# Optimization experiments

Hardware: AMD Instinct MI355X
Metric: run time of the kernel (lower is better)

## Reference

```python
import jax, jax.numpy as jnp
import numpy as np

N_NODES = 200000
N_EDGES = 6400000
IN_DIM, HID_DIM, OUT_DIM = 32, 32, 16


def setup_inputs() -> dict:
    key = jax.random.key(0)
    kx, ke, k1, k2, k3, k4 = jax.random.split(key, 6)
    x = jax.random.normal(kx, (N_NODES, IN_DIM), dtype=jnp.float32)
    edge_index = jax.random.randint(ke, (2, N_EDGES), 0, N_NODES, dtype=jnp.int32)
    # Glorot-ish init for GCNConv weights, zero bias (PyG default bias=True)
    W1 = jax.random.normal(k1, (IN_DIM, HID_DIM), dtype=jnp.float32) * (1.0 / np.sqrt(IN_DIM))
    b1 = jnp.zeros((HID_DIM,), dtype=jnp.float32)
    W2 = jax.random.normal(k2, (HID_DIM, OUT_DIM), dtype=jnp.float32) * (1.0 / np.sqrt(HID_DIM))
    b2 = jnp.zeros((OUT_DIM,), dtype=jnp.float32)
    return {"x": x, "edge_index": edge_index, "W1": W1, "b1": b1, "W2": W2, "b2": b2}


def reference(x, edge_index, W1, b1, W2, b2):
    n = x.shape[0]
    loops = jnp.arange(n, dtype=edge_index.dtype)
    # PyG GCNConv default: add self-loops, symmetric normalization
    src = jnp.concatenate([edge_index[0], loops])  # message source j
    dst = jnp.concatenate([edge_index[1], loops])  # aggregation target i
    deg = jax.ops.segment_sum(jnp.ones_like(dst, dtype=x.dtype), dst, num_segments=n)
    dinv = jax.lax.rsqrt(deg)  # deg >= 1 thanks to self-loops
    norm = dinv[src] * dinv[dst]  # [E+N]

    def gcn_conv(h, W, b):
        hw = h @ W                                   # [N, F_out] transform first (F_out <= F_in)
        msg = hw[src] * norm[:, None]                # [E+N, F_out] gather + scale
        return jax.ops.segment_sum(msg, dst, num_segments=n) + b

    h1 = jax.nn.relu(gcn_conv(x, W1, b1))
    # dropout p=0.0 is identity
    return gcn_conv(h1, W2, b2)
```

## Files before the change

### kernel.cpp

```cpp
#include <hip/hip_runtime.h>
#include <hip/hip_fp16.h>


#define BN 256
#define NBSZ 800
#define CHUNK 6144
#define KPT (CHUNK / 256)
#define CAPB 9216
#define CAP 12288
#define SRCCH 25000

typedef _Float16 h2f __attribute__((ext_vector_type(2)));

__device__ __forceinline__ h2f u2h(unsigned u) {
    union { unsigned u; h2f h; } x; x.u = u; return x.h;
}
__device__ __forceinline__ float fd2(h2f a, h2f sel, float acc) {
    return __builtin_amdgcn_fdot2(a, sel, acc, false);
}

__global__ __launch_bounds__(256) void init_cursors(int* gcursor, int nb) {
    int i = blockIdx.x * 256 + threadIdx.x;
    if (i < nb) gcursor[i] = i * CAPB;
}

__global__ __launch_bounds__(256) void partition_kernel(
    const int* __restrict__ src, const int* __restrict__ dst, int E,
    int* __restrict__ gcursor, unsigned int* __restrict__ ebuf, int nb) {
    __shared__ int hist[NBSZ];
    __shared__ int cur[NBSZ];
    __shared__ int gbase[NBSZ];
    __shared__ unsigned int sword[CHUNK];
    __shared__ unsigned short sbkt[CHUNK];
    __shared__ int wsum[4];
    __shared__ int totv;
    int tid = threadIdx.x;
    int e0 = blockIdx.x * CHUNK;
    int myd[KPT], mys[KPT];
    for (int k = 0; k < KPT; ++k) {
        int e = e0 + k * 256 + tid;
        myd[k] = (e < E) ? dst[e] : -1;
        mys[k] = (e < E) ? src[e] : 0;
    }
    for (int b = tid; b < nb; b += 256) hist[b] = 0;
    __syncthreads();
    for (int k = 0; k < KPT; ++k) if (myd[k] >= 0) atomicAdd(&hist[myd[k] >> 8], 1);
    __syncthreads();
    {
        int lane = tid & 63, wid = tid >> 6;
        int s0 = tid * 4;
        int local[4]; int part = 0;
        for (int j = 0; j < 4; ++j) { int b = s0 + j; local[j] = (b < nb) ? hist[b] : 0; part += local[j]; }
        int v = part;
        for (int o = 1; o < 64; o <<= 1) { int t = __shfl_up(v, o); if (lane >= o) v += t; }
        if (lane == 63) wsum[wid] = v;
        __syncthreads();
        int woff = 0;
        for (int w = 0; w < wid; ++w) woff += wsum[w];
        int run = woff + v - part;
        for (int j = 0; j < 4; ++j) {
            int b = s0 + j;
            if (b < nb) { hist[b] = run; cur[b] = run; run += local[j]; }
        }
        if (tid == 255) totv = run;
    }
    __syncthreads();
    for (int k = 0; k < KPT; ++k) {
        if (myd[k] >= 0) {
            int b = myd[k] >> 8;
            int r = atomicAdd(&cur[b], 1);
            sword[r] = ((unsigned)mys[k] << 8) | (unsigned)(myd[k] & 255);
            sbkt[r] = (unsigned short)b;
        }
    }
    __syncthreads();
    for (int b = tid; b < nb; b += 256) {
        int c = cur[b] - hist[b];
        if (c) gbase[b] = atomicAdd(&gcursor[b], c);
    }
    __syncthreads();
    int tv = totv;
    for (int i = tid; i < tv; i += 256) {
        int b = sbkt[i];
        ebuf[gbase[b] + (i - hist[b])] = sword[i];
    }
}

__global__ __launch_bounds__(256) void refine_kernel(
    unsigned int* __restrict__ ebuf, const int* __restrict__ gcursor,
    int* __restrict__ node_start, uint2* __restrict__ node_degc,
    float* __restrict__ dinv, int n) {
    __shared__ int cnt[BN * 8];
    __shared__ int cur[BN * 8];
    __shared__ int wsum[4];
    __shared__ int ssrc[CAP];
    int b = blockIdx.x, tid = threadIdx.x;
    int s = b * CAPB;
    int len = gcursor[b] - s;
    for (int i = tid; i < BN * 8; i += 256) cnt[i] = 0;
    __syncthreads();
    for (int i = tid; i < len; i += 256) {
        unsigned int w = ebuf[s + i];
        unsigned int key = ((w & 255u) << 3) | ((w >> 8) / SRCCH);
        atomicAdd(&cnt[key], 1);
    }
    __syncthreads();
    int s0 = tid * 8;
    int local[8]; int part = 0;
#pragma unroll
    for (int j = 0; j < 8; ++j) { local[j] = cnt[s0 + j]; part += local[j]; }
    int v = part;
    int lane = tid & 63, wid = tid >> 6;
    for (int o = 1; o < 64; o <<= 1) { int t = __shfl_up(v, o); if (lane >= o) v += t; }
    if (lane == 63) wsum[wid] = v;
    __syncthreads();
    int woff = 0;
    for (int w = 0; w < wid; ++w) woff += wsum[w];
    int run = woff + v - part;
    int mystart = run;
#pragma unroll
    for (int j = 0; j < 8; ++j) { cnt[s0 + j] = run; cur[s0 + j] = run; run += local[j]; }
    int node = b * BN + tid;
    if (node < n) {
        node_start[node] = s + mystart;
        uint2 dc;
        dc.x = (unsigned)local[0] | ((unsigned)local[1] << 8)
             | ((unsigned)local[2] << 16) | ((unsigned)local[3] << 24);
        dc.y = (unsigned)local[4] | ((unsigned)local[5] << 8)
             | ((unsigned)local[6] << 16) | ((unsigned)local[7] << 24);
        node_degc[node] = dc;
        dinv[node] = rsqrtf((float)part + 1.0f);
    }
    __syncthreads();
    if (len <= CAP) {
        for (int i = tid; i < len; i += 256) {
            unsigned int w = ebuf[s + i];
            unsigned int key = ((w & 255u) << 3) | ((w >> 8) / SRCCH);
            int r = atomicAdd(&cur[key], 1);
            ssrc[r] = (int)(w >> 8);
        }
        __syncthreads();
        for (int i = tid; i < len; i += 256) ebuf[s + i] = (unsigned int)ssrc[i];
    } else {
        for (int i = tid; i < len; i += 256) {
            unsigned int w = ebuf[s + i];
            unsigned int key = ((w & 255u) << 3) | ((w >> 8) / SRCCH);
            int r = atomicAdd(&cur[key], 1);
            ebuf[s + r] = (w >> 8);
        }
    }
}

__global__ __launch_bounds__(256) void transform1(
    const float* __restrict__ x, const float* __restrict__ W1,
    const float* __restrict__ dinv, __half* __restrict__ hws1, int n) {
    __shared__ float sW[32 * 32];
    __shared__ float sx[8 * 32];
    int tid = threadIdx.x;
    for (int i = tid; i < 1024; i += 256) sW[i] = W1[i];
    int node0 = blockIdx.x * 8;
    int node_ld = node0 + tid / 32;
    sx[tid] = (node_ld < n) ? x[node_ld * 32 + (tid & 31)] : 0.0f;
    __syncthreads();
    int local = tid >> 5;
    int f = tid & 31;
    int node = node0 + local;
    if (node >= n) return;
    float acc = 0.0f;
#pragma unroll
    for (int k = 0; k < 32; ++k) acc += sx[local * 32 + k] * sW[k * 32 + f];
    hws1[(size_t)node * 32 + f] = __float2half(acc * dinv[node]);
}

__global__ __launch_bounds__(256) void pull1_fused(
    const int* __restrict__ node_start, const uint2* __restrict__ node_degc,
    const unsigned int* __restrict__ ecsr, const float* __restrict__ dinv,
    const __half* __restrict__ hws1, const float* __restrict__ b1,
    const float* __restrict__ W2, __half* __restrict__ hws2, int n) {
    __shared__ float sW2[32 * 17];
    __shared__ float sb1[32];
    int tid = threadIdx.x;
    for (int i = tid; i < 512; i += 256) sW2[(i >> 4) * 17 + (i & 15)] = W2[i];
    if (tid < 32) sb1[tid] = b1[tid];
    __syncthreads();
    const h2f SEL_LO = {(_Float16)1.0f, (_Float16)0.0f};
    const h2f SEL_HI = {(_Float16)0.0f, (_Float16)1.0f};
    int g = tid >> 2;
    int l = tid & 3;
    int d = blockIdx.x * 64 + g;
    if (d >= n) return;
    int b = node_start[d];
    uint2 dc = node_degc[d];
    const char* Hb = (const char*)hws1;
    unsigned loff = (unsigned)(l << 4);
    float acc[8] = {0, 0, 0, 0, 0, 0, 0, 0};
    {
        uint4 r = *(const uint4*)(Hb + (((unsigned)d << 6) | loff));
        acc[0] = fd2(u2h(r.x), SEL_LO, acc[0]); acc[1] = fd2(u2h(r.x), SEL_HI, acc[1]);
        acc[2] = fd2(u2h(r.y), SEL_LO, acc[2]); acc[3] = fd2(u2h(r.y), SEL_HI, acc[3]);
        acc[4] = fd2(u2h(r.z), SEL_LO, acc[4]); acc[5] = fd2(u2h(r.z), SEL_HI, acc[5]);
        acc[6] = fd2(u2h(r.w), SEL_LO, acc[6]); acc[7] = fd2(u2h(r.w), SEL_HI, acc[7]);
    }
    int off = 0;
#pragma unroll
    for (int c = 0; c < 8; ++c) {
        unsigned int word = (c < 4) ? dc.x : dc.y;
        int lc = (int)((word >> (8 * (c & 3))) & 255u);
        int j = 0;
        for (; j + 4 <= lc; j += 4) {
            unsigned o0 = (ecsr[b + off + j]     << 6) | loff;
            unsigned o1 = (ecsr[b + off + j + 1] << 6) | loff;
            unsigned o2 = (ecsr[b + off + j + 2] << 6) | loff;
            unsigned o3 = (ecsr[b + off + j + 3] << 6) | loff;
            uint4 r0 = *(const uint4*)(Hb + o0);
            uint4 r1 = *(const uint4*)(Hb + o1);
            uint4 r2 = *(const uint4*)(Hb + o2);
            uint4 r3 = *(const uint4*)(Hb + o3);
            h2f sx = (u2h(r0.x) + u2h(r1.x)) + (u2h(r2.x) + u2h(r3.x));
            h2f sy = (u2h(r0.y) + u2h(r1.y)) + (u2h(r2.y) + u2h(r3.y));
            h2f sz = (u2h(r0.z) + u2h(r1.z)) + (u2h(r2.z) + u2h(r3.z));
            h2f sw = (u2h(r0.w) + u2h(r1.w)) + (u2h(r2.w) + u2h(r3.w));
            acc[0] = fd2(sx, SEL_LO, acc[0]); acc[1] = fd2(sx, SEL_HI, acc[1]);
            acc[2] = fd2(sy, SEL_LO, acc[2]); acc[3] = fd2(sy, SEL_HI, acc[3]);
            acc[4] = fd2(sz, SEL_LO, acc[4]); acc[5] = fd2(sz, SEL_HI, acc[5]);
            acc[6] = fd2(sw, SEL_LO, acc[6]); acc[7] = fd2(sw, SEL_HI, acc[7]);
        }
        for (; j < lc; ++j) {
            uint4 r = *(const uint4*)(Hb + ((ecsr[b + off + j] << 6) | loff));
            acc[0] = fd2(u2h(r.x), SEL_LO, acc[0]); acc[1] = fd2(u2h(r.x), SEL_HI, acc[1]);
            acc[2] = fd2(u2h(r.y), SEL_LO, acc[2]); acc[3] = fd2(u2h(r.y), SEL_HI, acc[3]);
            acc[4] = fd2(u2h(r.z), SEL_LO, acc[4]); acc[5] = fd2(u2h(r.z), SEL_HI, acc[5]);
            acc[6] = fd2(u2h(r.w), SEL_LO, acc[6]); acc[7] = fd2(u2h(r.w), SEL_HI, acc[7]);
        }
        off += lc;
    }
    float di = dinv[d];
    float h1v[8];
#pragma unroll
    for (int q = 0; q < 8; ++q)
        h1v[q] = fmaxf(sb1[8 * l + q] + di * acc[q], 0.0f);
    float p[16];
#pragma unroll
    for (int f = 0; f < 16; ++f) p[f] = 0.0f;
#pragma unroll
    for (int q = 0; q < 8; ++q) {
        float hv = h1v[q];
        const float* wrow = &sW2[(8 * l + q) * 17];
#pragma unroll
        for (int f = 0; f < 16; ++f) p[f] += hv * wrow[f];
    }
#pragma unroll
    for (int f = 0; f < 16; ++f) {
        p[f] += __shfl_xor(p[f], 1);
        p[f] += __shfl_xor(p[f], 2);
    }
    __half2 o0 = __floats2half2_rn(p[4 * l] * di, p[4 * l + 1] * di);
    __half2 o1 = __floats2half2_rn(p[4 * l + 2] * di, p[4 * l + 3] * di);
    __half2* HW2 = (__half2*)hws2;
    HW2[(size_t)d * 8 + 2 * l]     = o0;
    HW2[(size_t)d * 8 + 2 * l + 1] = o1;
}

__global__ __launch_bounds__(256) void pull2(
    const int* __restrict__ node_start, const uint2* __restrict__ node_degc,
    const unsigned int* __restrict__ ecsr, const float* __restrict__ dinv,
    const __half* __restrict__ hws2, const float* __restrict__ b2,
    float* __restrict__ out, int n) {
    const h2f SEL_LO = {(_Float16)1.0f, (_Float16)0.0f};
    const h2f SEL_HI = {(_Float16)0.0f, (_Float16)1.0f};
    int g = threadIdx.x >> 2;
    int l = threadIdx.x & 3;
    int d = blockIdx.x * 64 + g;
    if (d >= n) return;
    int b = node_start[d];
    uint2 dc = node_degc[d];
    const char* Hb = (const char*)hws2;
    unsigned loff = (unsigned)(l << 3);
    float acc[4] = {0, 0, 0, 0};
    {
        uint2 r = *(const uint2*)(Hb + (((unsigned)d << 5) | loff));
        acc[0] = fd2(u2h(r.x), SEL_LO, acc[0]); acc[1] = fd2(u2h(r.x), SEL_HI, acc[1]);
        acc[2] = fd2(u2h(r.y), SEL_LO, acc[2]); acc[3] = fd2(u2h(r.y), SEL_HI, acc[3]);
    }
    int off = 0;
#pragma unroll
    for (int c = 0; c < 4; ++c) {
        unsigned int word = (c < 2) ? dc.x : dc.y;
        int sh = 16 * (c & 1);
        int lc = (int)((word >> sh) & 255u) + (int)((word >> (sh + 8)) & 255u);
        int j = 0;
        for (; j + 4 <= lc; j += 4) {
            unsigned o0 = (ecsr[b + off + j]     << 5) | loff;
            unsigned o1 = (ecsr[b + off + j + 1] << 5) | loff;
            unsigned o2 = (ecsr[b + off + j + 2] << 5) | loff;
            unsigned o3 = (ecsr[b + off + j + 3] << 5) | loff;
            uint2 w0 = *(const uint2*)(Hb + o0);
            uint2 w1 = *(const uint2*)(Hb + o1);
            uint2 w2 = *(const uint2*)(Hb + o2);
            uint2 w3 = *(const uint2*)(Hb + o3);
            h2f sx = (u2h(w0.x) + u2h(w1.x)) + (u2h(w2.x) + u2h(w3.x));
            h2f sy = (u2h(w0.y) + u2h(w1.y)) + (u2h(w2.y) + u2h(w3.y));
            acc[0] = fd2(sx, SEL_LO, acc[0]); acc[1] = fd2(sx, SEL_HI, acc[1]);
            acc[2] = fd2(sy, SEL_LO, acc[2]); acc[3] = fd2(sy, SEL_HI, acc[3]);
        }
        for (; j < lc; ++j) {
            uint2 w0 = *(const uint2*)(Hb + ((ecsr[b + off + j] << 5) | loff));
            acc[0] = fd2(u2h(w0.x), SEL_LO, acc[0]); acc[1] = fd2(u2h(w0.x), SEL_HI, acc[1]);
            acc[2] = fd2(u2h(w0.y), SEL_LO, acc[2]); acc[3] = fd2(u2h(w0.y), SEL_HI, acc[3]);
        }
        off += lc;
    }
    float di = dinv[d];
    float4 o;
    o.x = b2[4 * l + 0] + di * acc[0];
    o.y = b2[4 * l + 1] + di * acc[1];
    o.z = b2[4 * l + 2] + di * acc[2];
    o.w = b2[4 * l + 3] + di * acc[3];
    ((float4*)out)[(size_t)d * 4 + l] = o;
}

extern "C" void kernel_launch(void* const* d_in, const int* in_sizes, int n_in,
                              void* d_out, int out_size, void* d_ws, size_t ws_size,
                              hipStream_t stream) {
    const float* x  = (const float*)d_in[0];
    const int*   ei = (const int*)d_in[1];
    const float* W1 = (const float*)d_in[2];
    const float* b1 = (const float*)d_in[3];
    const float* W2 = (const float*)d_in[4];
    const float* b2 = (const float*)d_in[5];

    int n = in_sizes[0] / 32;
    int E = in_sizes[1] / 2;
    const int* src = ei;
    const int* dst = ei + E;

    int nb = (n + BN - 1) / BN;

    char* w = (char*)d_ws;
    int*   gcursor     = (int*)w;    w += (size_t)NBSZ * 4;
    float* dinv        = (float*)w;  w += (size_t)n * 4;
    int*   node_start  = (int*)w;    w += (size_t)n * 4;
    uint2* node_degc   = (uint2*)w;  w += (size_t)n * 8;
    unsigned int* ebuf = (unsigned int*)w; w += (size_t)nb * CAPB * 4;
    __half* hws1       = (__half*)w; w += (size_t)n * 32 * 2;
    __half* hws2       = (__half*)w; w += (size_t)n * 16 * 2;
    float* out         = (float*)d_out;

    int nchunks = (E + CHUNK - 1) / CHUNK;

    init_cursors    <<<(nb + 255) / 256, 256, 0, stream>>>(gcursor, nb);
    partition_kernel<<<nchunks, 256, 0, stream>>>(src, dst, E, gcursor, ebuf, nb);
    refine_kernel   <<<nb, 256, 0, stream>>>(ebuf, gcursor, node_start, node_degc, dinv, n);

    transform1 <<<(n + 7) / 8, 256, 0, stream>>>(x, W1, dinv, hws1, n);
    pull1_fused<<<(n + 63) / 64, 256, 0, stream>>>(node_start, node_degc, ebuf, dinv,
                                                   hws1, b1, W2, hws2, n);
    pull2      <<<(n + 63) / 64, 256, 0, stream>>>(node_start, node_degc, ebuf, dinv,
                                                   hws2, b2, out, n);
}
```

Measured before the change: 261.2 us.

## Pad CSR sub-buckets to multiples of four with dummy zero-row indices

Each per-node, per-source-chunk edge segment is rounded up to a multiple of four and padded with index n, which points to a zeroed extra row appended to the fp16 feature buffers. The pull kernels then load four indices with a single 16-byte load and drop their scalar remainder loops. The refine kernel always sorts through shared memory, now sized to the larger bucket capacity. In exchange, the pull kernels do extra gathers of the zero row and the edge buffer grows; the larger shared array may also lower refine-kernel occupancy.

```diff
diff --git a/kernel.cpp b/kernel.cpp
--- a/kernel.cpp
+++ b/kernel.cpp
@@ -6,8 +6,7 @@
 #define NBSZ 800
 #define CHUNK 6144
 #define KPT (CHUNK / 256)
-#define CAPB 9216
-#define CAP 12288
+#define CAPB 12288
 #define SRCCH 25000
 
 typedef _Float16 h2f __attribute__((ext_vector_type(2)));
@@ -19,9 +18,14 @@
     return __builtin_amdgcn_fdot2(a, sel, acc, false);
 }
 
-__global__ __launch_bounds__(256) void init_cursors(int* gcursor, int nb) {
+__global__ __launch_bounds__(256) void setup_kernel(int* gcursor, int nb,
+                                                    __half* hws1, __half* hws2, int n) {
     int i = blockIdx.x * 256 + threadIdx.x;
     if (i < nb) gcursor[i] = i * CAPB;
+    if (blockIdx.x == 0) {
+        if (threadIdx.x < 32) hws1[(size_t)n * 32 + threadIdx.x] = __float2half(0.0f);
+        if (threadIdx.x < 16) hws2[(size_t)n * 16 + threadIdx.x] = __float2half(0.0f);
+    }
 }
 
 __global__ __launch_bounds__(256) void partition_kernel(
@@ -93,7 +97,7 @@
     __shared__ int cnt[BN * 8];
     __shared__ int cur[BN * 8];
     __shared__ int wsum[4];
-    __shared__ int ssrc[CAP];
+    __shared__ int ssrc[CAPB];
     int b = blockIdx.x, tid = threadIdx.x;
     int s = b * CAPB;
     int len = gcursor[b] - s;
@@ -106,49 +110,51 @@
     }
     __syncthreads();
     int s0 = tid * 8;
-    int local[8]; int part = 0;
-#pragma unroll
-    for (int j = 0; j < 8; ++j) { local[j] = cnt[s0 + j]; part += local[j]; }
-    int v = part;
+    int localp[8]; int part = 0; int ppart = 0;
+#pragma unroll
+    for (int j = 0; j < 8; ++j) {
+        int c = cnt[s0 + j];
+        part += c;
+        localp[j] = (c + 3) & ~3;
+        ppart += localp[j];
+    }
+    int v = ppart;
     int lane = tid & 63, wid = tid >> 6;
     for (int o = 1; o < 64; o <<= 1) { int t = __shfl_up(v, o); if (lane >= o) v += t; }
     if (lane == 63) wsum[wid] = v;
     __syncthreads();
     int woff = 0;
     for (int w = 0; w < wid; ++w) woff += wsum[w];
-    int run = woff + v - part;
+    int run = woff + v - ppart;
     int mystart = run;
 #pragma unroll
-    for (int j = 0; j < 8; ++j) { cnt[s0 + j] = run; cur[s0 + j] = run; run += local[j]; }
+    for (int j = 0; j < 8; ++j) { cur[s0 + j] = run; run += localp[j]; }
+    int plen_my = run;
     int node = b * BN + tid;
     if (node < n) {
         node_start[node] = s + mystart;
         uint2 dc;
-        dc.x = (unsigned)local[0] | ((unsigned)local[1] << 8)
-             | ((unsigned)local[2] << 16) | ((unsigned)local[3] << 24);
-        dc.y = (unsigned)local[4] | ((unsigned)local[5] << 8)
-             | ((unsigned)local[6] << 16) | ((unsigned)local[7] << 24);
+        dc.x = (unsigned)localp[0] | ((unsigned)localp[1] << 8)
+             | ((unsigned)localp[2] << 16) | ((unsigned)localp[3] << 24);
+        dc.y = (unsigned)localp[4] | ((unsigned)localp[5] << 8)
+             | ((unsigned)localp[6] << 16) | ((unsigned)localp[7] << 24);
         node_degc[node] = dc;
         dinv[node] = rsqrtf((float)part + 1.0f);
     }
-    __syncthreads();
-    if (len <= CAP) {
-        for (int i = tid; i < len; i += 256) {
-            unsigned int w = ebuf[s + i];
-            unsigned int key = ((w & 255u) << 3) | ((w >> 8) / SRCCH);
-            int r = atomicAdd(&cur[key], 1);
-            ssrc[r] = (int)(w >> 8);
-        }
-        __syncthreads();
-        for (int i = tid; i < len; i += 256) ebuf[s + i] = (unsigned int)ssrc[i];
-    } else {
-        for (int i = tid; i < len; i += 256) {
-            unsigned int w = ebuf[s + i];
-            unsigned int key = ((w & 255u) << 3) | ((w >> 8) / SRCCH);
-            int r = atomicAdd(&cur[key], 1);
-            ebuf[s + r] = (w >> 8);
-        }
-    }
+    __shared__ int plen_s;
+    if (tid == 255) plen_s = plen_my;
+    __syncthreads();
+    int plen = plen_s;
+    for (int i = tid; i < plen; i += 256) ssrc[i] = n;
+    __syncthreads();
+    for (int i = tid; i < len; i += 256) {
+        unsigned int w = ebuf[s + i];
+        unsigned int key = ((w & 255u) << 3) | ((w >> 8) / SRCCH);
+        int r = atomicAdd(&cur[key], 1);
+        ssrc[r] = (int)(w >> 8);
+    }
+    __syncthreads();
+    for (int i = tid; i < plen; i += 256) ebuf[s + i] = (unsigned int)ssrc[i];
 }
 
 __global__ __launch_bounds__(256) void transform1(
@@ -206,16 +212,12 @@
     for (int c = 0; c < 8; ++c) {
         unsigned int word = (c < 4) ? dc.x : dc.y;
         int lc = (int)((word >> (8 * (c & 3))) & 255u);
-        int j = 0;
-        for (; j + 4 <= lc; j += 4) {
-            unsigned o0 = (ecsr[b + off + j]     << 6) | loff;
-            unsigned o1 = (ecsr[b + off + j + 1] << 6) | loff;
-            unsigned o2 = (ecsr[b + off + j + 2] << 6) | loff;
-            unsigned o3 = (ecsr[b + off + j + 3] << 6) | loff;
-            uint4 r0 = *(const uint4*)(Hb + o0);
-            uint4 r1 = *(const uint4*)(Hb + o1);
-            uint4 r2 = *(const uint4*)(Hb + o2);
-            uint4 r3 = *(const uint4*)(Hb + o3);
+        for (int j = 0; j < lc; j += 4) {
+            uint4 idx = *(const uint4*)(ecsr + b + off + j);
+            uint4 r0 = *(const uint4*)(Hb + ((idx.x << 6) | loff));
+            uint4 r1 = *(const uint4*)(Hb + ((idx.y << 6) | loff));
+            uint4 r2 = *(const uint4*)(Hb + ((idx.z << 6) | loff));
+            uint4 r3 = *(const uint4*)(Hb + ((idx.w << 6) | loff));
             h2f sx = (u2h(r0.x) + u2h(r1.x)) + (u2h(r2.x) + u2h(r3.x));
             h2f sy = (u2h(r0.y) + u2h(r1.y)) + (u2h(r2.y) + u2h(r3.y));
             h2f sz = (u2h(r0.z) + u2h(r1.z)) + (u2h(r2.z) + u2h(r3.z));
@@ -224,13 +226,6 @@
             acc[2] = fd2(sy, SEL_LO, acc[2]); acc[3] = fd2(sy, SEL_HI, acc[3]);
             acc[4] = fd2(sz, SEL_LO, acc[4]); acc[5] = fd2(sz, SEL_HI, acc[5]);
             acc[6] = fd2(sw, SEL_LO, acc[6]); acc[7] = fd2(sw, SEL_HI, acc[7]);
-        }
-        for (; j < lc; ++j) {
-            uint4 r = *(const uint4*)(Hb + ((ecsr[b + off + j] << 6) | loff));
-            acc[0] = fd2(u2h(r.x), SEL_LO, acc[0]); acc[1] = fd2(u2h(r.x), SEL_HI, acc[1]);
-            acc[2] = fd2(u2h(r.y), SEL_LO, acc[2]); acc[3] = fd2(u2h(r.y), SEL_HI, acc[3]);
-            acc[4] = fd2(u2h(r.z), SEL_LO, acc[4]); acc[5] = fd2(u2h(r.z), SEL_HI, acc[5]);
-            acc[6] = fd2(u2h(r.w), SEL_LO, acc[6]); acc[7] = fd2(u2h(r.w), SEL_HI, acc[7]);
         }
         off += lc;
     }
@@ -288,25 +283,16 @@
         unsigned int word = (c < 2) ? dc.x : dc.y;
         int sh = 16 * (c & 1);
         int lc = (int)((word >> sh) & 255u) + (int)((word >> (sh + 8)) & 255u);
-        int j = 0;
-        for (; j + 4 <= lc; j += 4) {
-            unsigned o0 = (ecsr[b + off + j]     << 5) | loff;
-            unsigned o1 = (ecsr[b + off + j + 1] << 5) | loff;
-            unsigned o2 = (ecsr[b + off + j + 2] << 5) | loff;
-            unsigned o3 = (ecsr[b + off + j + 3] << 5) | loff;
-            uint2 w0 = *(const uint2*)(Hb + o0);
-            uint2 w1 = *(const uint2*)(Hb + o1);
-            uint2 w2 = *(const uint2*)(Hb + o2);
-            uint2 w3 = *(const uint2*)(Hb + o3);
+        for (int j = 0; j < lc; j += 4) {
+            uint4 idx = *(const uint4*)(ecsr + b + off + j);
+            uint2 w0 = *(const uint2*)(Hb + ((idx.x << 5) | loff));
+            uint2 w1 = *(const uint2*)(Hb + ((idx.y << 5) | loff));
+            uint2 w2 = *(const uint2*)(Hb + ((idx.z << 5) | loff));
+            uint2 w3 = *(const uint2*)(Hb + ((idx.w << 5) | loff));
             h2f sx = (u2h(w0.x) + u2h(w1.x)) + (u2h(w2.x) + u2h(w3.x));
             h2f sy = (u2h(w0.y) + u2h(w1.y)) + (u2h(w2.y) + u2h(w3.y));
             acc[0] = fd2(sx, SEL_LO, acc[0]); acc[1] = fd2(sx, SEL_HI, acc[1]);
             acc[2] = fd2(sy, SEL_LO, acc[2]); acc[3] = fd2(sy, SEL_HI, acc[3]);
-        }
-        for (; j < lc; ++j) {
-            uint2 w0 = *(const uint2*)(Hb + ((ecsr[b + off + j] << 5) | loff));
-            acc[0] = fd2(u2h(w0.x), SEL_LO, acc[0]); acc[1] = fd2(u2h(w0.x), SEL_HI, acc[1]);
-            acc[2] = fd2(u2h(w0.y), SEL_LO, acc[2]); acc[3] = fd2(u2h(w0.y), SEL_HI, acc[3]);
         }
         off += lc;
     }
@@ -342,13 +328,13 @@
     int*   node_start  = (int*)w;    w += (size_t)n * 4;
     uint2* node_degc   = (uint2*)w;  w += (size_t)n * 8;
     unsigned int* ebuf = (unsigned int*)w; w += (size_t)nb * CAPB * 4;
-    __half* hws1       = (__half*)w; w += (size_t)n * 32 * 2;
-    __half* hws2       = (__half*)w; w += (size_t)n * 16 * 2;
+    __half* hws1       = (__half*)w; w += (size_t)(n + 1) * 32 * 2;
+    __half* hws2       = (__half*)w; w += (size_t)(n + 1) * 16 * 2;
     float* out         = (float*)d_out;
 
     int nchunks = (E + CHUNK - 1) / CHUNK;
 
-    init_cursors    <<<(nb + 255) / 256, 256, 0, stream>>>(gcursor, nb);
+    setup_kernel    <<<(nb + 255) / 256, 256, 0, stream>>>(gcursor, nb, hws1, hws2, n);
     partition_kernel<<<nchunks, 256, 0, stream>>>(src, dst, E, gcursor, ebuf, nb);
     refine_kernel   <<<nb, 256, 0, stream>>>(ebuf, gcursor, node_start, node_degc, dinv, n);
 
```

Result: slower. 299.1 us (+14.5%).
